# Optimization experiments

Hardware: AMD Instinct MI355X
Metric: run time of the kernel (lower is better)

The kernel has to match this reference:

```python
import jax, jax.numpy as jnp
import numpy as np

N, E, D, NUM_REL, NUM_LAYERS = 20000, 100000, 768, 7, 5  # 6 edge types + self-loop relation


def setup_inputs() -> dict:
    key = jax.random.key(0)
    ks = jax.random.split(key, 8)
    x = jax.random.normal(ks[0], (N, D), dtype=jnp.float32)
    edge_index = jax.random.randint(ks[1], (2, E), 0, N, dtype=jnp.int64)
    # original edge_type values are in [-1, 5]; module adds 1 -> [0, 6]
    edge_type = jax.random.randint(ks[2], (E,), -1, 6, dtype=jnp.int64)
    scale = 1.0 / np.sqrt(D)
    weights = jax.random.normal(ks[3], (NUM_LAYERS, NUM_REL, D, D), dtype=jnp.float32) * scale
    roots = jax.random.normal(ks[4], (NUM_LAYERS, D, D), dtype=jnp.float32) * scale
    biases = jax.random.normal(ks[5], (NUM_LAYERS, D), dtype=jnp.float32) * 0.01
    return {"x": x, "edge_index": edge_index, "edge_type": edge_type,
            "weights": weights, "roots": roots, "biases": biases}


def _rgcn_conv(h, src, dst, safe_et, W, root, b):
    # PyG RGCNConv (aggr='mean', root_weight=True, bias=True):
    #   out = x @ root + b + sum_r mean_{edges of rel r into v}(x[src]) @ W_r
    n = h.shape[0]
    hs = h[src]  # [E, D] gather once, reused across relations
    out = h @ root + b
    for r in range(NUM_REL):
        m = (safe_et == r).astype(h.dtype)  # [E]
        msg_sum = jax.ops.segment_sum(hs * m[:, None], dst, num_segments=n)  # [N, D]
        cnt = jax.ops.segment_sum(m, dst, num_segments=n)  # [N]
        mean = msg_sum / jnp.maximum(cnt, 1.0)[:, None]  # zero where no rel-r edges
        out = out + mean @ W[r]
    return out


def reference(x, edge_index, edge_type, weights, roots, biases):
    src, dst = edge_index[0], edge_index[1]
    safe_et = edge_type + 1  # [-1..5] -> [0..6]
    h = x
    for l in range(NUM_LAYERS):
        h = _rgcn_conv(h, src, dst, safe_et, weights[l], roots[l], biases[l])
        h = jax.nn.relu(h)  # dropout=0 -> identity
    return h
```

## Files before the change

kernel.cpp:

```cpp
#include <hip/hip_runtime.h>

typedef unsigned short u16;
typedef unsigned int   u32;
typedef __attribute__((ext_vector_type(8))) short short8;
typedef __attribute__((ext_vector_type(4))) float f32x4;

#define DD      768
#define KK      6144
#define NREL    7
#define NLAYERS 5

__device__ __forceinline__ float b2f(u16 v) {
  return __uint_as_float(((u32)v) << 16);
}
__device__ __forceinline__ u16 f2bf(float f) {
  u32 x = __float_as_uint(f);
  x += 0x7fffu + ((x >> 16) & 1u);
  return (u16)(x >> 16);
}
__device__ __forceinline__ void gload16(const void* g, void* l) {
  __builtin_amdgcn_global_load_lds(
      (const __attribute__((address_space(1))) void*)g,
      (__attribute__((address_space(3))) void*)l, 16, 0, 0);
}


__global__ void cast_x_kernel(const float* __restrict__ x, u16* __restrict__ H, size_t n) {
  for (size_t i = ((size_t)blockIdx.x * 256 + threadIdx.x) * 4; i < n; i += (size_t)gridDim.x * 256 * 4) {
    float4 v = *(const float4*)&x[i];
    u32 lo = (u32)f2bf(v.x) | ((u32)f2bf(v.y) << 16);
    u32 hi = (u32)f2bf(v.z) | ((u32)f2bf(v.w) << 16);
    uint2 o; o.x = lo; o.y = hi;
    *(uint2*)&H[i] = o;
  }
}

__global__ void count_kernel(const int* __restrict__ eidx, const int* __restrict__ etype,
                             int* cnt_dst, int* cnt_rel, int E, int Nn) {
  int e = blockIdx.x * 256 + threadIdx.x;
  if (e >= E) return;
  int dst = eidx[E + e];
  int rel = etype[e] + 1;
  atomicAdd(&cnt_dst[dst], 1);
  atomicAdd(&cnt_rel[(size_t)rel * Nn + dst], 1);
}

__global__ __launch_bounds__(1024) void scan_kernel(const int* __restrict__ cnt, int* __restrict__ offs, int n) {
  __shared__ int part[1024];
  int t = threadIdx.x;
  int per = (n + 1023) / 1024;
  int base = t * per;
  int s = 0;
  for (int i = 0; i < per; ++i) { int idx = base + i; if (idx < n) s += cnt[idx]; }
  part[t] = s;
  __syncthreads();
  for (int o = 1; o < 1024; o <<= 1) {
    int v = (t >= o) ? part[t - o] : 0;
    __syncthreads();
    part[t] += v;
    __syncthreads();
  }
  int excl = (t == 0) ? 0 : part[t - 1];
  s = excl;
  for (int i = 0; i < per; ++i) { int idx = base + i; if (idx < n) { offs[idx] = s; s += cnt[idx]; } }
  if (t == 1023) offs[n] = part[1023];
}

__global__ void fillperm_kernel(const int* __restrict__ eidx, const int* __restrict__ offs,
                                int* fill, int* perm, int E) {
  int e = blockIdx.x * 256 + threadIdx.x;
  if (e >= E) return;
  int dst = eidx[E + e];
  int pos = offs[dst] + atomicAdd(&fill[dst], 1);
  perm[pos] = e;
}

__global__ void wcat_kernel(const float* __restrict__ W, const float* __restrict__ R, u16* __restrict__ Bt) {
  __shared__ float t[32 * 33];
  int b = blockIdx.x;
  int s = b / 576, rem = b % 576;
  int kt = rem / 24, nt = rem % 24;
  const float* src = (s == 0) ? R : (W + (size_t)(s - 1) * DD * DD);
  int tj = threadIdx.x & 31, ti = threadIdx.x >> 5;
#pragma unroll
  for (int i = 0; i < 4; ++i) {
    int kk = kt * 32 + ti + i * 8;
    t[(ti + i * 8) * 33 + tj] = src[(size_t)kk * DD + nt * 32 + tj];
  }
  __syncthreads();
#pragma unroll
  for (int i = 0; i < 4; ++i) {
    int nn_ = nt * 32 + ti + i * 8;
    Bt[(size_t)nn_ * KK + (size_t)s * DD + kt * 32 + tj] = f2bf(t[tj * 33 + ti + i * 8]);
  }
}

__global__ void copy_h_kernel(const u16* __restrict__ Hin, u16* __restrict__ Acat, int nn) {
  size_t total = (size_t)nn * (DD / 8);
  for (size_t i = (size_t)blockIdx.x * 256 + threadIdx.x; i < total; i += (size_t)gridDim.x * 256) {
    size_t r = i / (DD / 8), c = i % (DD / 8);
    *(uint4*)&Acat[r * KK + c * 8] = *(const uint4*)&Hin[r * DD + c * 8];
  }
}

__global__ __launch_bounds__(192) void aggregate_kernel(
    const u16* __restrict__ H, const int* __restrict__ esrc, const int* __restrict__ etype,
    const int* __restrict__ offs, const int* __restrict__ perm, const int* __restrict__ cnt_rel,
    u16* __restrict__ Acat, int node0, int Nn) {
  int v = node0 + blockIdx.x;
  int t = threadIdx.x;
  int j0 = t * 4;
  float a0[4] = {0,0,0,0}, a1[4] = {0,0,0,0}, a2[4] = {0,0,0,0}, a3[4] = {0,0,0,0};
  float a4[4] = {0,0,0,0}, a5[4] = {0,0,0,0}, a6[4] = {0,0,0,0};
  int beg = offs[v], end = offs[v + 1];
  for (int e = beg; e < end; ++e) {
    int eid = perm[e];
    int src = esrc[eid];
    int rel = etype[eid] + 1;
    uint2 w = *(const uint2*)&H[(size_t)src * DD + j0];
    float f0 = b2f((u16)(w.x & 0xffff));
    float f1 = b2f((u16)(w.x >> 16));
    float f2 = b2f((u16)(w.y & 0xffff));
    float f3 = b2f((u16)(w.y >> 16));
    switch (rel) {
      case 0: a0[0]+=f0; a0[1]+=f1; a0[2]+=f2; a0[3]+=f3; break;
      case 1: a1[0]+=f0; a1[1]+=f1; a1[2]+=f2; a1[3]+=f3; break;
      case 2: a2[0]+=f0; a2[1]+=f1; a2[2]+=f2; a2[3]+=f3; break;
      case 3: a3[0]+=f0; a3[1]+=f1; a3[2]+=f2; a3[3]+=f3; break;
      case 4: a4[0]+=f0; a4[1]+=f1; a4[2]+=f2; a4[3]+=f3; break;
      case 5: a5[0]+=f0; a5[1]+=f1; a5[2]+=f2; a5[3]+=f3; break;
      default: a6[0]+=f0; a6[1]+=f1; a6[2]+=f2; a6[3]+=f3; break;
    }
  }
  size_t rowbase = (size_t)blockIdx.x * KK;
  const float* regs[NREL] = {a0, a1, a2, a3, a4, a5, a6};
#pragma unroll
  for (int r = 0; r < NREL; ++r) {
    int c = cnt_rel[(size_t)r * Nn + v];
    float inv = (c > 0) ? 1.f / (float)c : 0.f;
    const float* a = regs[r];
    u32 lo = (u32)f2bf(a[0] * inv) | ((u32)f2bf(a[1] * inv) << 16);
    u32 hi = (u32)f2bf(a[2] * inv) | ((u32)f2bf(a[3] * inv) << 16);
    uint2 o; o.x = lo; o.y = hi;
    *(uint2*)&Acat[rowbase + (size_t)(r + 1) * DD + j0] = o;
  }
}


__global__ __launch_bounds__(512, 2) void gemm256_kernel(
    const u16* __restrict__ A, const u16* __restrict__ Bt, const float* __restrict__ bias,
    u16* __restrict__ Hout, float* __restrict__ Cout, int Mvalid, int Mtiles) {
  __shared__ u16 sm[4][16384];

  int tid = threadIdx.x;
  int lane = tid & 63;
  int wv = tid >> 6;
  int wm = wv >> 2, wn = wv & 3;

  int nwg = Mtiles * 3;
  int orig = (int)blockIdx.x;
  int q8 = nwg >> 3, r8 = nwg & 7;
  int xcd = orig & 7, rank = orig >> 3;
  int wg = (xcd < r8 ? xcd * (q8 + 1) : r8 * (q8 + 1) + (xcd - r8) * q8) + rank;
  int bm = wg / 3, bn = wg % 3;

  const char* gA[2];
  const char* gB[2];
#pragma unroll
  for (int j = 0; j < 2; ++j) {
    int qq = j * 8192 + tid * 16;
    int qp = qq ^ (((qq >> 9) & 1) << 5);
    int row = ((qp >> 10) << 4) | ((qp >> 6) & 15);
    int kb  = qp & 63;
    gA[j] = (const char*)A  + (size_t)(bm * 256 + row) * (KK * 2) + kb;
    gB[j] = (const char*)Bt + (size_t)(bn * 256 + row) * (KK * 2) + kb;
  }
  int rsel = lane & 15;
  int laneoff = ((rsel * 64) + ((lane >> 4) * 16)) ^ ((rsel & 8) << 2);

  f32x4 acc[8][4];
#pragma unroll
  for (int m = 0; m < 8; ++m)
#pragma unroll
    for (int n = 0; n < 4; ++n) acc[m][n] = (f32x4){0.f, 0.f, 0.f, 0.f};

  const int NSTEP = KK / 32;

#define STAGE(t2)                                                        \
  do {                                                                   \
    int s_ = (t2) & 3;                                                   \
    size_t ko_ = (size_t)(t2) * 64;                                      \
    char* d_ = (char*)&sm[s_][0];                                        \
    gload16(gA[0] + ko_, d_ + tid * 16);                                 \
    gload16(gA[1] + ko_, d_ + 8192 + tid * 16);                          \
    gload16(gB[0] + ko_, d_ + 16384 + tid * 16);                         \
    gload16(gB[1] + ko_, d_ + 16384 + 8192 + tid * 16);                  \
  } while (0)

#define READF(t2, ar, br)                                                \
  do {                                                                   \
    const char* base_ = (const char*)&sm[(t2) & 3][0];                   \
    _Pragma("unroll")                                                    \
    for (int m = 0; m < 8; ++m)                                          \
      ar[m] = *(const short8*)(base_ + (wm * 8 + m) * 1024 + laneoff);   \
    _Pragma("unroll")                                                    \
    for (int n = 0; n < 4; ++n)                                          \
      br[n] = *(const short8*)(base_ + 16384 + (wn * 4 + n) * 1024 + laneoff); \
  } while (0)

#define MFMA32(ar, br)                                                   \
  do {                                                                   \
    _Pragma("unroll")                                                    \
    for (int m = 0; m < 8; ++m)                                          \
      _Pragma("unroll")                                                  \
      for (int n = 0; n < 4; ++n)                                        \
        acc[m][n] = __builtin_amdgcn_mfma_f32_16x16x32_bf16(ar[m], br[n], acc[m][n], 0, 0, 0); \
  } while (0)

  short8 aE[8], bE[4], aO[8], bO[4];

  STAGE(0); STAGE(1); STAGE(2);
  asm volatile("s_waitcnt vmcnt(4)" ::: "memory");
  __builtin_amdgcn_s_barrier();
  __builtin_amdgcn_sched_barrier(0);
  READF(0, aE, bE);

  for (int t = 0; t < NSTEP; t += 2) {
    if (t + 3 < NSTEP) STAGE(t + 3);
    READF(t + 1, aO, bO);
    __builtin_amdgcn_sched_barrier(0);
    __builtin_amdgcn_s_setprio(1);
    MFMA32(aE, bE);
    __builtin_amdgcn_s_setprio(0);
    asm volatile("s_waitcnt vmcnt(4)" ::: "memory");
    __builtin_amdgcn_s_barrier();
    __builtin_amdgcn_sched_barrier(0);

    if (t + 4 < NSTEP) STAGE(t + 4);
    if (t + 2 < NSTEP) READF(t + 2, aE, bE);
    __builtin_amdgcn_sched_barrier(0);
    __builtin_amdgcn_s_setprio(1);
    MFMA32(aO, bO);
    __builtin_amdgcn_s_setprio(0);
    asm volatile("s_waitcnt vmcnt(4)" ::: "memory");
    __builtin_amdgcn_s_barrier();
    __builtin_amdgcn_sched_barrier(0);
  }
#undef STAGE
#undef READF
#undef MFMA32

  int rif = (lane >> 4) * 4;
  int cidx = lane & 15;
#pragma unroll
  for (int m = 0; m < 8; ++m) {
    int rl = bm * 256 + wm * 128 + m * 16 + rif;
#pragma unroll
    for (int n = 0; n < 4; ++n) {
      int c = bn * 256 + wn * 64 + n * 16 + cidx;
      float bv = bias[c];
#pragma unroll
      for (int j = 0; j < 4; ++j) {
        int r = rl + j;
        if (r < Mvalid) {
          float v = acc[m][n][j] + bv;
          v = v > 0.f ? v : 0.f;
          if (Hout) Hout[(size_t)r * DD + c] = f2bf(v);
          if (Cout) Cout[(size_t)r * DD + c] = v;
        }
      }
    }
  }
}


static inline size_t alignup(size_t x, size_t a) { return (x + a - 1) & ~(a - 1); }

extern "C" void kernel_launch(void* const* d_in, const int* in_sizes, int n_in,
                              void* d_out, int out_size, void* d_ws, size_t ws_size,
                              hipStream_t stream) {
  const float* x       = (const float*)d_in[0];
  const int*   eidx    = (const int*)d_in[1];
  const int*   etype   = (const int*)d_in[2];
  const float* weights = (const float*)d_in[3];
  const float* roots   = (const float*)d_in[4];
  const float* biases  = (const float*)d_in[5];
  float* out = (float*)d_out;

  const int Nn = in_sizes[0] / DD;
  const int E  = in_sizes[2];

  char* p = (char*)d_ws;
  size_t off = 0;
  auto carve = [&](size_t bytes) -> char* {
    char* r = p + off;
    off = alignup(off + bytes, 256);
    return r;
  };
  u16* H0      = (u16*)carve((size_t)Nn * DD * 2);
  u16* Bt      = (u16*)carve((size_t)DD * KK * 2);
  int* cnt_rel = (int*)carve((size_t)NREL * Nn * 4);
  int* cnt_dst = (int*)carve((size_t)Nn * 4);
  int* offs    = (int*)carve((size_t)(Nn + 1) * 4);
  int* fill    = (int*)carve((size_t)Nn * 4);
  int* perm    = (int*)carve((size_t)E * 4);

  size_t rem = (ws_size > off) ? (ws_size - off) : 0;
  int McCap = (int)(rem / ((size_t)KK * 2));
  int Mpad = ((Nn + 255) / 256) * 256;
  int Mc = (McCap < Mpad) ? (McCap & ~255) : Mpad;
  if (Mc < 256) return;
  u16* Acat = (u16*)(p + off);
  int nchunks = (Nn + Mc - 1) / Mc;
  u16* H1 = (u16*)d_out;

  (void)hipMemsetAsync(cnt_rel, 0, (size_t)NREL * Nn * 4, stream);
  (void)hipMemsetAsync(cnt_dst, 0, (size_t)Nn * 4, stream);
  (void)hipMemsetAsync(fill, 0, (size_t)Nn * 4, stream);

  int eg = (E + 255) / 256;
  count_kernel<<<eg, 256, 0, stream>>>(eidx, etype, cnt_dst, cnt_rel, E, Nn);
  scan_kernel<<<1, 1024, 0, stream>>>(cnt_dst, offs, Nn);
  fillperm_kernel<<<eg, 256, 0, stream>>>(eidx, offs, fill, perm, E);
  cast_x_kernel<<<2048, 256, 0, stream>>>(x, H0, (size_t)Nn * DD);

  const u16* Hin = H0;
  u16* Hnext = H1;
  for (int l = 0; l < NLAYERS; ++l) {
    wcat_kernel<<<8 * 576, 256, 0, stream>>>(weights + (size_t)l * NREL * DD * DD,
                                             roots + (size_t)l * DD * DD, Bt);
    for (int c = 0; c < nchunks; ++c) {
      int node0 = c * Mc;
      int nn = (Nn - node0 < Mc) ? (Nn - node0) : Mc;
      int copy16 = nn * (DD / 8);
      int cb = (copy16 + 255) / 256;
      if (cb > 2048) cb = 2048;
      copy_h_kernel<<<cb, 256, 0, stream>>>(Hin + (size_t)node0 * DD, Acat, nn);
      aggregate_kernel<<<nn, 192, 0, stream>>>(Hin, eidx, etype, offs, perm, cnt_rel,
                                               Acat, node0, Nn);
      int mt = (nn + 255) / 256;
      u16* ho = (l < NLAYERS - 1) ? (Hnext + (size_t)node0 * DD) : nullptr;
      float* co = (l == NLAYERS - 1) ? (out + (size_t)node0 * DD) : nullptr;
      gemm256_kernel<<<mt * 3, 512, 0, stream>>>(Acat, Bt, biases + (size_t)l * DD, ho, co, nn, mt);
    }
    const u16* t_ = Hin;
    Hin = Hnext;
    Hnext = (u16*)t_;
  }
}
```

Measured before the change: 1.482 ms.

## Interleave LDS reads and global prefetch with MFMA chunks; fuse self-copy into aggregate

The GEMM main loop is rewritten so each half-step splits its 32 MFMAs into four groups of 8. Between the groups it issues the LDS fragment reads for the next step and one global-to-LDS prefetch, instead of doing all loads before the MFMA block. The goal is to hide LDS and global-load latency behind matrix work. Separately, the copy of each node's own features into the concatenated A matrix is folded into the aggregate kernel, which removes one kernel launch and a separate pass over memory. Near the end of K the prefetch index is clamped, so a few redundant loads are issued; the register lifetimes also become more complex.

```diff
diff --git a/kernel.cpp b/kernel.cpp
--- a/kernel.cpp
+++ b/kernel.cpp
@@ -95,14 +95,6 @@
   }
 }
 
-__global__ void copy_h_kernel(const u16* __restrict__ Hin, u16* __restrict__ Acat, int nn) {
-  size_t total = (size_t)nn * (DD / 8);
-  for (size_t i = (size_t)blockIdx.x * 256 + threadIdx.x; i < total; i += (size_t)gridDim.x * 256) {
-    size_t r = i / (DD / 8), c = i % (DD / 8);
-    *(uint4*)&Acat[r * KK + c * 8] = *(const uint4*)&Hin[r * DD + c * 8];
-  }
-}
-
 __global__ __launch_bounds__(192) void aggregate_kernel(
     const u16* __restrict__ H, const int* __restrict__ esrc, const int* __restrict__ etype,
     const int* __restrict__ offs, const int* __restrict__ perm, const int* __restrict__ cnt_rel,
@@ -110,6 +102,8 @@
   int v = node0 + blockIdx.x;
   int t = threadIdx.x;
   int j0 = t * 4;
+  size_t rowbase = (size_t)blockIdx.x * KK;
+  *(uint2*)&Acat[rowbase + j0] = *(const uint2*)&H[(size_t)v * DD + j0];
   float a0[4] = {0,0,0,0}, a1[4] = {0,0,0,0}, a2[4] = {0,0,0,0}, a3[4] = {0,0,0,0};
   float a4[4] = {0,0,0,0}, a5[4] = {0,0,0,0}, a6[4] = {0,0,0,0};
   int beg = offs[v], end = offs[v + 1];
@@ -132,7 +126,6 @@
       default: a6[0]+=f0; a6[1]+=f1; a6[2]+=f2; a6[3]+=f3; break;
     }
   }
-  size_t rowbase = (size_t)blockIdx.x * KK;
   const float* regs[NREL] = {a0, a1, a2, a3, a4, a5, a6};
 #pragma unroll
   for (int r = 0; r < NREL; ++r) {
@@ -186,7 +179,10 @@
 
   const int NSTEP = KK / 32;
 
-#define STAGE(t2)                                                        \
+#define RD_A(base_, r_)  (*(const short8*)((base_) + (r_) * 1024 + laneoff))
+#define RD_B(base_, r_)  (*(const short8*)((base_) + 16384 + (r_) * 1024 + laneoff))
+
+#define STAGE_FULL(t2)                                                   \
   do {                                                                   \
     int s_ = (t2) & 3;                                                   \
     size_t ko_ = (size_t)(t2) * 64;                                      \
@@ -197,58 +193,83 @@
     gload16(gB[1] + ko_, d_ + 16384 + 8192 + tid * 16);                  \
   } while (0)
 
-#define READF(t2, ar, br)                                                \
-  do {                                                                   \
-    const char* base_ = (const char*)&sm[(t2) & 3][0];                   \
-    _Pragma("unroll")                                                    \
-    for (int m = 0; m < 8; ++m)                                          \
-      ar[m] = *(const short8*)(base_ + (wm * 8 + m) * 1024 + laneoff);   \
-    _Pragma("unroll")                                                    \
-    for (int n = 0; n < 4; ++n)                                          \
-      br[n] = *(const short8*)(base_ + 16384 + (wn * 4 + n) * 1024 + laneoff); \
-  } while (0)
-
-#define MFMA32(ar, br)                                                   \
+#define MFMA8(AR, BR, M0)                                                \
   do {                                                                   \
     _Pragma("unroll")                                                    \
-    for (int m = 0; m < 8; ++m)                                          \
-      _Pragma("unroll")                                                  \
-      for (int n = 0; n < 4; ++n)                                        \
-        acc[m][n] = __builtin_amdgcn_mfma_f32_16x16x32_bf16(ar[m], br[n], acc[m][n], 0, 0, 0); \
+    for (int n_ = 0; n_ < 4; ++n_) {                                     \
+      acc[(M0)][n_]     = __builtin_amdgcn_mfma_f32_16x16x32_bf16(AR[(M0)],     BR[n_], acc[(M0)][n_],     0, 0, 0); \
+      acc[(M0) + 1][n_] = __builtin_amdgcn_mfma_f32_16x16x32_bf16(AR[(M0) + 1], BR[n_], acc[(M0) + 1][n_], 0, 0, 0); \
+    }                                                                    \
   } while (0)
 
+#define HALF(tcur, AC, BC, AN, BN_)                                      \
+  do {                                                                   \
+    const char* rb_ = (const char*)&sm[((tcur) + 1) & 3][0];             \
+    int tc_ = (tcur) + 3;                                                \
+    int ts_ = tc_ & 3;                                                   \
+    int tk_ = tc_ < NSTEP ? tc_ : NSTEP - 1;                             \
+    size_t ko_ = (size_t)tk_ * 64;                                       \
+    char* sd_ = (char*)&sm[ts_][0];                                      \
+    __builtin_amdgcn_s_setprio(1);                                       \
+    MFMA8(AC, BC, 0);                                                    \
+    __builtin_amdgcn_sched_barrier(0);                                   \
+    AN[0] = RD_A(rb_, wm * 8 + 0);                                       \
+    AN[1] = RD_A(rb_, wm * 8 + 1);                                       \
+    AN[2] = RD_A(rb_, wm * 8 + 2);                                       \
+    gload16(gA[0] + ko_, sd_ + tid * 16);                                \
+    __builtin_amdgcn_sched_barrier(0);                                   \
+    MFMA8(AC, BC, 2);                                                    \
+    __builtin_amdgcn_sched_barrier(0);                                   \
+    AN[3] = RD_A(rb_, wm * 8 + 3);                                       \
+    AN[4] = RD_A(rb_, wm * 8 + 4);                                       \
+    AN[5] = RD_A(rb_, wm * 8 + 5);                                       \
+    gload16(gA[1] + ko_, sd_ + 8192 + tid * 16);                         \
+    __builtin_amdgcn_sched_barrier(0);                                   \
+    MFMA8(AC, BC, 4);                                                    \
+    __builtin_amdgcn_sched_barrier(0);                                   \
+    AN[6] = RD_A(rb_, wm * 8 + 6);                                       \
+    AN[7] = RD_A(rb_, wm * 8 + 7);                                       \
+    BN_[0] = RD_B(rb_, wn * 4 + 0);                                      \
+    gload16(gB[0] + ko_, sd_ + 16384 + tid * 16);                        \
+    __builtin_amdgcn_sched_barrier(0);                                   \
+    MFMA8(AC, BC, 6);                                                    \
+    __builtin_amdgcn_sched_barrier(0);                                   \
+    BN_[1] = RD_B(rb_, wn * 4 + 1);                                      \
+    BN_[2] = RD_B(rb_, wn * 4 + 2);                                      \
+    BN_[3] = RD_B(rb_, wn * 4 + 3);                                      \
+    gload16(gB[1] + ko_, sd_ + 16384 + 8192 + tid * 16);                 \
+    __builtin_amdgcn_s_setprio(0);                                       \
+    asm volatile("s_waitcnt vmcnt(4)" ::: "memory");                     \
+    __builtin_amdgcn_s_barrier();                                        \
+    __builtin_amdgcn_sched_barrier(0);                                   \
+  } while (0)
+
   short8 aE[8], bE[4], aO[8], bO[4];
 
-  STAGE(0); STAGE(1); STAGE(2);
+  STAGE_FULL(0); STAGE_FULL(1); STAGE_FULL(2);
   asm volatile("s_waitcnt vmcnt(4)" ::: "memory");
   __builtin_amdgcn_s_barrier();
   __builtin_amdgcn_sched_barrier(0);
-  READF(0, aE, bE);
-
-  for (int t = 0; t < NSTEP; t += 2) {
-    if (t + 3 < NSTEP) STAGE(t + 3);
-    READF(t + 1, aO, bO);
-    __builtin_amdgcn_sched_barrier(0);
-    __builtin_amdgcn_s_setprio(1);
-    MFMA32(aE, bE);
-    __builtin_amdgcn_s_setprio(0);
-    asm volatile("s_waitcnt vmcnt(4)" ::: "memory");
-    __builtin_amdgcn_s_barrier();
-    __builtin_amdgcn_sched_barrier(0);
-
-    if (t + 4 < NSTEP) STAGE(t + 4);
-    if (t + 2 < NSTEP) READF(t + 2, aE, bE);
-    __builtin_amdgcn_sched_barrier(0);
-    __builtin_amdgcn_s_setprio(1);
-    MFMA32(aO, bO);
-    __builtin_amdgcn_s_setprio(0);
-    asm volatile("s_waitcnt vmcnt(4)" ::: "memory");
-    __builtin_amdgcn_s_barrier();
-    __builtin_amdgcn_sched_barrier(0);
-  }
-#undef STAGE
-#undef READF
-#undef MFMA32
+#pragma unroll
+  for (int m = 0; m < 8; ++m) aE[m] = RD_A((const char*)&sm[0][0], wm * 8 + m);
+#pragma unroll
+  for (int n = 0; n < 4; ++n) bE[n] = RD_B((const char*)&sm[0][0], wn * 4 + n);
+  __builtin_amdgcn_sched_barrier(0);
+
+  for (int t = 0; t < NSTEP - 2; t += 2) {
+    HALF(t,     aE, bE, aO, bO);
+    HALF(t + 1, aO, bO, aE, bE);
+  }
+  HALF(NSTEP - 2, aE, bE, aO, bO);
+  __builtin_amdgcn_s_setprio(1);
+  MFMA8(aO, bO, 0); MFMA8(aO, bO, 2); MFMA8(aO, bO, 4); MFMA8(aO, bO, 6);
+  __builtin_amdgcn_s_setprio(0);
+
+#undef HALF
+#undef MFMA8
+#undef STAGE_FULL
+#undef RD_A
+#undef RD_B
 
   int rif = (lane >> 4) * 4;
   int cidx = lane & 15;
@@ -332,10 +353,6 @@
     for (int c = 0; c < nchunks; ++c) {
       int node0 = c * Mc;
       int nn = (Nn - node0 < Mc) ? (Nn - node0) : Mc;
-      int copy16 = nn * (DD / 8);
-      int cb = (copy16 + 255) / 256;
-      if (cb > 2048) cb = 2048;
-      copy_h_kernel<<<cb, 256, 0, stream>>>(Hin + (size_t)node0 * DD, Acat, nn);
       aggregate_kernel<<<nn, 192, 0, stream>>>(Hin, eidx, etype, offs, perm, cnt_rel,
                                                Acat, node0, Nn);
       int mt = (nn + 255) / 256;
```

Result: faster. 1.424 ms (-3.9%).

## Fold root-row copy into aggregation and shrink GEMM tile to 128x256

Applied to the files above, without the earlier changes.

Removes the separate copy_h kernel by having each aggregation block write its own node's feature row into the concatenated A matrix. The GEMM moves from a 256x256 tile with a 4-stage LDS ring to a 128x256 tile with 3-stage buffering, smaller accumulators and a new LDS swizzle. A-row loads are clamped to the last valid row so padding rows are never read. This gives more workgroups across the CUs for N=20000 and higher occupancy, at the cost of lower arithmetic intensity per tile and more B traffic.

```diff
diff --git a/kernel.cpp b/kernel.cpp
--- a/kernel.cpp
+++ b/kernel.cpp
@@ -95,14 +95,6 @@
   }
 }
 
-__global__ void copy_h_kernel(const u16* __restrict__ Hin, u16* __restrict__ Acat, int nn) {
-  size_t total = (size_t)nn * (DD / 8);
-  for (size_t i = (size_t)blockIdx.x * 256 + threadIdx.x; i < total; i += (size_t)gridDim.x * 256) {
-    size_t r = i / (DD / 8), c = i % (DD / 8);
-    *(uint4*)&Acat[r * KK + c * 8] = *(const uint4*)&Hin[r * DD + c * 8];
-  }
-}
-
 __global__ __launch_bounds__(192) void aggregate_kernel(
     const u16* __restrict__ H, const int* __restrict__ esrc, const int* __restrict__ etype,
     const int* __restrict__ offs, const int* __restrict__ perm, const int* __restrict__ cnt_rel,
@@ -110,6 +102,8 @@
   int v = node0 + blockIdx.x;
   int t = threadIdx.x;
   int j0 = t * 4;
+  size_t rowbase = (size_t)blockIdx.x * KK;
+  *(uint2*)&Acat[rowbase + j0] = *(const uint2*)&H[(size_t)v * DD + j0];
   float a0[4] = {0,0,0,0}, a1[4] = {0,0,0,0}, a2[4] = {0,0,0,0}, a3[4] = {0,0,0,0};
   float a4[4] = {0,0,0,0}, a5[4] = {0,0,0,0}, a6[4] = {0,0,0,0};
   int beg = offs[v], end = offs[v + 1];
@@ -132,7 +126,6 @@
       default: a6[0]+=f0; a6[1]+=f1; a6[2]+=f2; a6[3]+=f3; break;
     }
   }
-  size_t rowbase = (size_t)blockIdx.x * KK;
   const float* regs[NREL] = {a0, a1, a2, a3, a4, a5, a6};
 #pragma unroll
   for (int r = 0; r < NREL; ++r) {
@@ -147,10 +140,13 @@
 }
 
 
-__global__ __launch_bounds__(512, 2) void gemm256_kernel(
+#define MFMA_(a_, b_, c_) __builtin_amdgcn_mfma_f32_16x16x32_bf16(a_, b_, c_, 0, 0, 0)
+
+__global__ __launch_bounds__(512, 4) void gemm128_kernel(
     const u16* __restrict__ A, const u16* __restrict__ Bt, const float* __restrict__ bias,
     u16* __restrict__ Hout, float* __restrict__ Cout, int Mvalid, int Mtiles) {
-  __shared__ u16 sm[4][16384];
+  __shared__ u16 smA[3][128 * 32];
+  __shared__ u16 smB[3][256 * 32];
 
   int tid = threadIdx.x;
   int lane = tid & 63;
@@ -164,97 +160,72 @@
   int wg = (xcd < r8 ? xcd * (q8 + 1) : r8 * (q8 + 1) + (xcd - r8) * q8) + rank;
   int bm = wg / 3, bn = wg % 3;
 
-  const char* gA[2];
-  const char* gB[2];
-#pragma unroll
-  for (int j = 0; j < 2; ++j) {
-    int qq = j * 8192 + tid * 16;
-    int qp = qq ^ (((qq >> 9) & 1) << 5);
-    int row = ((qp >> 10) << 4) | ((qp >> 6) & 15);
-    int kb  = qp & 63;
-    gA[j] = (const char*)A  + (size_t)(bm * 256 + row) * (KK * 2) + kb;
-    gB[j] = (const char*)Bt + (size_t)(bn * 256 + row) * (KK * 2) + kb;
-  }
-  int rsel = lane & 15;
-  int laneoff = ((rsel * 64) + ((lane >> 4) * 16)) ^ ((rsel & 8) << 2);
-
-  f32x4 acc[8][4];
-#pragma unroll
-  for (int m = 0; m < 8; ++m)
+  int srow = tid >> 2;
+  int schunk = (tid & 3) ^ ((tid >> 3) & 3);
+  int ra = bm * 128 + srow; if (ra > Mvalid - 1) ra = Mvalid - 1;
+  const char* gA  = (const char*)A  + (size_t)ra * (KK * 2) + schunk * 16;
+  const char* gB0 = (const char*)Bt + (size_t)(bn * 256 + srow) * (KK * 2) + schunk * 16;
+  const char* gB1 = gB0 + (size_t)128 * (KK * 2);
+
+  int rsel = lane & 15, kq = lane >> 4;
+  int loff = rsel * 64 + ((kq ^ ((rsel >> 1) & 3)) * 16);
+
+  f32x4 acc[4][4];
+#pragma unroll
+  for (int m = 0; m < 4; ++m)
 #pragma unroll
     for (int n = 0; n < 4; ++n) acc[m][n] = (f32x4){0.f, 0.f, 0.f, 0.f};
 
   const int NSTEP = KK / 32;
 
-#define STAGE(t2)                                                        \
+#define STAGE(t2, slot)                                                  \
   do {                                                                   \
-    int s_ = (t2) & 3;                                                   \
     size_t ko_ = (size_t)(t2) * 64;                                      \
-    char* d_ = (char*)&sm[s_][0];                                        \
-    gload16(gA[0] + ko_, d_ + tid * 16);                                 \
-    gload16(gA[1] + ko_, d_ + 8192 + tid * 16);                          \
-    gload16(gB[0] + ko_, d_ + 16384 + tid * 16);                         \
-    gload16(gB[1] + ko_, d_ + 16384 + 8192 + tid * 16);                  \
+    gload16(gA + ko_,  (char*)&smA[slot][0] + tid * 16);                 \
+    gload16(gB0 + ko_, (char*)&smB[slot][0] + tid * 16);                 \
+    gload16(gB1 + ko_, (char*)&smB[slot][0] + 8192 + tid * 16);          \
   } while (0)
 
-#define READF(t2, ar, br)                                                \
+#define KSTEP(tt, cur, nxt)                                              \
   do {                                                                   \
-    const char* base_ = (const char*)&sm[(t2) & 3][0];                   \
+    if ((tt) + 2 < NSTEP) STAGE((tt) + 2, nxt);                          \
+    const char* aB_ = (const char*)&smA[cur][0] + wm * 4096 + loff;      \
+    const char* bB_ = (const char*)&smB[cur][0] + wn * 4096 + loff;      \
+    short8 af_[4], bf_[4];                                               \
     _Pragma("unroll")                                                    \
-    for (int m = 0; m < 8; ++m)                                          \
-      ar[m] = *(const short8*)(base_ + (wm * 8 + m) * 1024 + laneoff);   \
+    for (int m_ = 0; m_ < 4; ++m_) af_[m_] = *(const short8*)(aB_ + m_ * 1024); \
     _Pragma("unroll")                                                    \
-    for (int n = 0; n < 4; ++n)                                          \
-      br[n] = *(const short8*)(base_ + 16384 + (wn * 4 + n) * 1024 + laneoff); \
+    for (int n_ = 0; n_ < 4; ++n_) bf_[n_] = *(const short8*)(bB_ + n_ * 1024); \
+    __builtin_amdgcn_s_setprio(1);                                       \
+    _Pragma("unroll")                                                    \
+    for (int m_ = 0; m_ < 4; ++m_)                                       \
+      _Pragma("unroll")                                                  \
+      for (int n_ = 0; n_ < 4; ++n_)                                     \
+        acc[m_][n_] = MFMA_(af_[m_], bf_[n_], acc[m_][n_]);              \
+    __builtin_amdgcn_s_setprio(0);                                       \
+    if ((tt) + 2 < NSTEP) asm volatile("s_waitcnt vmcnt(3)" ::: "memory"); \
+    else                  asm volatile("s_waitcnt vmcnt(0)" ::: "memory"); \
+    __builtin_amdgcn_s_barrier();                                        \
   } while (0)
 
-#define MFMA32(ar, br)                                                   \
-  do {                                                                   \
-    _Pragma("unroll")                                                    \
-    for (int m = 0; m < 8; ++m)                                          \
-      _Pragma("unroll")                                                  \
-      for (int n = 0; n < 4; ++n)                                        \
-        acc[m][n] = __builtin_amdgcn_mfma_f32_16x16x32_bf16(ar[m], br[n], acc[m][n], 0, 0, 0); \
-  } while (0)
-
-  short8 aE[8], bE[4], aO[8], bO[4];
-
-  STAGE(0); STAGE(1); STAGE(2);
-  asm volatile("s_waitcnt vmcnt(4)" ::: "memory");
+  STAGE(0, 0);
+  STAGE(1, 1);
+  asm volatile("s_waitcnt vmcnt(3)" ::: "memory");
   __builtin_amdgcn_s_barrier();
-  __builtin_amdgcn_sched_barrier(0);
-  READF(0, aE, bE);
-
-  for (int t = 0; t < NSTEP; t += 2) {
-    if (t + 3 < NSTEP) STAGE(t + 3);
-    READF(t + 1, aO, bO);
-    __builtin_amdgcn_sched_barrier(0);
-    __builtin_amdgcn_s_setprio(1);
-    MFMA32(aE, bE);
-    __builtin_amdgcn_s_setprio(0);
-    asm volatile("s_waitcnt vmcnt(4)" ::: "memory");
-    __builtin_amdgcn_s_barrier();
-    __builtin_amdgcn_sched_barrier(0);
-
-    if (t + 4 < NSTEP) STAGE(t + 4);
-    if (t + 2 < NSTEP) READF(t + 2, aE, bE);
-    __builtin_amdgcn_sched_barrier(0);
-    __builtin_amdgcn_s_setprio(1);
-    MFMA32(aO, bO);
-    __builtin_amdgcn_s_setprio(0);
-    asm volatile("s_waitcnt vmcnt(4)" ::: "memory");
-    __builtin_amdgcn_s_barrier();
-    __builtin_amdgcn_sched_barrier(0);
-  }
+
+  for (int t = 0; t < NSTEP; t += 3) {
+    KSTEP(t,     0, 2);
+    KSTEP(t + 1, 1, 0);
+    KSTEP(t + 2, 2, 1);
+  }
+#undef KSTEP
 #undef STAGE
-#undef READF
-#undef MFMA32
 
   int rif = (lane >> 4) * 4;
   int cidx = lane & 15;
 #pragma unroll
-  for (int m = 0; m < 8; ++m) {
-    int rl = bm * 256 + wm * 128 + m * 16 + rif;
+  for (int m = 0; m < 4; ++m) {
+    int rl = bm * 128 + wm * 64 + m * 16 + rif;
 #pragma unroll
     for (int n = 0; n < 4; ++n) {
       int c = bn * 256 + wn * 64 + n * 16 + cidx;
@@ -307,9 +278,9 @@
 
   size_t rem = (ws_size > off) ? (ws_size - off) : 0;
   int McCap = (int)(rem / ((size_t)KK * 2));
-  int Mpad = ((Nn + 255) / 256) * 256;
-  int Mc = (McCap < Mpad) ? (McCap & ~255) : Mpad;
-  if (Mc < 256) return;
+  int Mpad = ((Nn + 127) / 128) * 128;
+  int Mc = (McCap < Mpad) ? (McCap & ~127) : Mpad;
+  if (Mc < 128) return;
   u16* Acat = (u16*)(p + off);
   int nchunks = (Nn + Mc - 1) / Mc;
   u16* H1 = (u16*)d_out;
@@ -332,16 +303,12 @@
     for (int c = 0; c < nchunks; ++c) {
       int node0 = c * Mc;
       int nn = (Nn - node0 < Mc) ? (Nn - node0) : Mc;
-      int copy16 = nn * (DD / 8);
-      int cb = (copy16 + 255) / 256;
-      if (cb > 2048) cb = 2048;
-      copy_h_kernel<<<cb, 256, 0, stream>>>(Hin + (size_t)node0 * DD, Acat, nn);
       aggregate_kernel<<<nn, 192, 0, stream>>>(Hin, eidx, etype, offs, perm, cnt_rel,
                                                Acat, node0, Nn);
-      int mt = (nn + 255) / 256;
+      int mt = (nn + 127) / 128;
       u16* ho = (l < NLAYERS - 1) ? (Hnext + (size_t)node0 * DD) : nullptr;
       float* co = (l == NLAYERS - 1) ? (out + (size_t)node0 * DD) : nullptr;
-      gemm256_kernel<<<mt * 3, 512, 0, stream>>>(Acat, Bt, biases + (size_t)l * DD, ho, co, nn, mt);
+      gemm128_kernel<<<mt * 3, 512, 0, stream>>>(Acat, Bt, biases + (size_t)l * DD, ho, co, nn, mt);
     }
     const u16* t_ = Hin;
     Hin = Hnext;
```

New measurement: 1.583 ms. 1.07x slower.
